# Optimization experiments

Measured on AMD Instinct MI355X. Metric: run time of the kernel, lower is better.

Reference implementation:

```python
import jax, jax.numpy as jnp
import numpy as np
import math

B, T, C, H = 2, 2048, 1024, 16
D = C // H

def setup_inputs() -> dict:
    key = jax.random.key(0)
    ks = jax.random.split(key, 10)
    s = 1.0 / math.sqrt(C)
    return {
        "x": jax.random.normal(ks[0], (B, T, C), jnp.float32),
        "x_query": jax.random.normal(ks[1], (B, T, C), jnp.float32),
        "Wq": jax.random.normal(ks[2], (C, C), jnp.float32) * s,
        "bq": jax.random.normal(ks[3], (C,), jnp.float32) * 0.02,
        "Wk": jax.random.normal(ks[4], (C, C), jnp.float32) * s,
        "bk": jax.random.normal(ks[5], (C,), jnp.float32) * 0.02,
        "Wv": jax.random.normal(ks[6], (C, C), jnp.float32) * s,
        "bv": jax.random.normal(ks[7], (C,), jnp.float32) * 0.02,
        "Wp": jax.random.normal(ks[8], (C, C), jnp.float32) * s,
        "bp": jax.random.normal(ks[9], (C,), jnp.float32) * 0.02,
    }

def reference(x, x_query, Wq, bq, Wk, bk, Wv, bv, Wp, bp):
    # torch nn.Linear: y = x @ W^T + b
    Tq = x_query.shape[1]
    Tk = x.shape[1]
    q = (x_query @ Wq.T + bq).reshape(B, Tq, H, D).transpose(0, 2, 1, 3)  # [B,H,Tq,D]
    k = (x @ Wk.T + bk).reshape(B, Tk, H, D).transpose(0, 2, 1, 3)       # [B,H,Tk,D]
    v = (x @ Wv.T + bv).reshape(B, Tk, H, D).transpose(0, 2, 1, 3)       # [B,H,Tk,D]
    scale = 1.0 / math.sqrt(D)
    att = jnp.einsum('bhqd,bhkd->bhqk', q, k) * scale                    # [B,H,Tq,Tk]
    # use_mask=True, past_kv=None -> causal tril mask over (Tq, Tk)
    mask = jnp.tril(jnp.ones((Tq, Tk), dtype=bool))
    att = jnp.where(mask[None, None, :, :], att, -jnp.inf)
    att = jax.nn.softmax(att, axis=-1)
    y = jnp.einsum('bhqk,bhkd->bhqd', att, v)                            # [B,H,Tq,D]
    y = y.transpose(0, 2, 1, 3).reshape(B, Tq, C)
    y = y @ Wp.T + bp
    return y
```

## Files before the change

### kernel.cpp

```cpp
#include <hip/hip_runtime.h>

typedef __bf16 bf16;
typedef __attribute__((ext_vector_type(8))) __bf16 bf16x8;
typedef __attribute__((ext_vector_type(4))) float f32x4;
typedef __attribute__((ext_vector_type(16))) float f32x16;
typedef __attribute__((ext_vector_type(4))) unsigned u32x4;

#define MFMA16(a, b, c) __builtin_amdgcn_mfma_f32_16x16x32_bf16((a), (b), (c), 0, 0, 0)
#define MFMA32(a, b, c) __builtin_amdgcn_mfma_f32_32x32x16_bf16((a), (b), (c), 0, 0, 0)
#define NEG_BIG (-1e30f)
#define SCL_LOG2 0.18033688011112042f

__device__ __forceinline__ void gload_lds16(void* lds, const void* g) {
  __builtin_amdgcn_global_load_lds(
      (const __attribute__((address_space(1))) void*)g,
      (__attribute__((address_space(3))) void*)lds, 16, 0, 0);
}

__device__ __forceinline__ unsigned pk2(float x, float y) {
  const unsigned short a = __builtin_bit_cast(unsigned short, (bf16)x);
  const unsigned short b = __builtin_bit_cast(unsigned short, (bf16)y);
  return (unsigned)a | ((unsigned)b << 16);
}

__global__ void cvt6(const float* __restrict__ s0, const float* __restrict__ s1,
                     const float* __restrict__ s2, const float* __restrict__ s3,
                     const float* __restrict__ s4, const float* __restrict__ s5,
                     bf16* __restrict__ d0, bf16* __restrict__ d1,
                     bf16* __restrict__ d2, bf16* __restrict__ d3,
                     bf16* __restrict__ d4, bf16* __restrict__ d5) {
  const int c = blockIdx.x * blockDim.x + threadIdx.x;
  if (c >= 1572864) return;
  const float* s; bf16* d; int off;
  if (c < 524288)        { s = s0; d = d0; off = c; }
  else if (c < 1048576)  { s = s1; d = d1; off = c - 524288; }
  else {
    const int c2 = c - 1048576, seg = c2 >> 17;
    off = c2 & 131071;
    s = seg == 0 ? s2 : seg == 1 ? s3 : seg == 2 ? s4 : s5;
    d = seg == 0 ? d2 : seg == 1 ? d3 : seg == 2 ? d4 : d5;
  }
  const float4 a = ((const float4*)s)[off * 2 + 0];
  const float4 b = ((const float4*)s)[off * 2 + 1];
  bf16x8 o;
  o[0] = (bf16)a.x; o[1] = (bf16)a.y; o[2] = (bf16)a.z; o[3] = (bf16)a.w;
  o[4] = (bf16)b.x; o[5] = (bf16)b.y; o[6] = (bf16)b.z; o[7] = (bf16)b.w;
  ((bf16x8*)d)[off] = o;
}

__global__ void gemm_qkv(const bf16* __restrict__ XQ, const bf16* __restrict__ X,
                         const bf16* __restrict__ Wq, const bf16* __restrict__ Wk,
                         const bf16* __restrict__ Wv,
                         const float* __restrict__ bq, const float* __restrict__ bk,
                         const float* __restrict__ bv,
                         bf16* __restrict__ Qo, bf16* __restrict__ Ko,
                         bf16* __restrict__ Vto) {
  __shared__ __align__(16) bf16 As[128 * 32];
  __shared__ __align__(16) bf16 Bs[128 * 32];
  const int tid = threadIdx.x;
  const int wv = tid >> 6, lane = tid & 63;
  const int wr = wv >> 1, wc = wv & 1;
  const int lr = lane & 15, lg = lane >> 4;
  const int seg = blockIdx.x >> 3;
  const int n0 = (blockIdx.x & 7) * 128;
  const int m0 = blockIdx.y * 128;
  const bf16* __restrict__ A = seg == 0 ? XQ : X;
  const bf16* __restrict__ W = seg == 0 ? Wq : seg == 1 ? Wk : Wv;
  const float* __restrict__ bias = seg == 0 ? bq : seg == 1 ? bk : bv;
  const int K = 1024;

  f32x4 acc[4][4] = {};

  for (int k0 = 0; k0 < K; k0 += 32) {
    __syncthreads();
#pragma unroll
    for (int j = 0; j < 2; ++j) {
      const int e8 = (j * 256 + tid) * 8;
      const int row = e8 >> 5, col = e8 & 31;
      gload_lds16(As + (size_t)(j * 256 + wv * 64) * 8,
                  A + (size_t)(m0 + row) * K + k0 + col);
      gload_lds16(Bs + (size_t)(j * 256 + wv * 64) * 8,
                  W + (size_t)(n0 + row) * K + k0 + col);
    }
    __syncthreads();
    bf16x8 af[4], bfr[4];
#pragma unroll
    for (int i = 0; i < 4; ++i)
      af[i] = *(const bf16x8*)&As[(wr * 64 + i * 16 + lr) * 32 + lg * 8];
#pragma unroll
    for (int j = 0; j < 4; ++j)
      bfr[j] = *(const bf16x8*)&Bs[(wc * 64 + j * 16 + lr) * 32 + lg * 8];
#pragma unroll
    for (int i = 0; i < 4; ++i)
#pragma unroll
      for (int j = 0; j < 4; ++j)
        acc[i][j] = MFMA16(af[i], bfr[j], acc[i][j]);
  }

#pragma unroll
  for (int j = 0; j < 4; ++j) {
    const int n = n0 + wc * 64 + j * 16 + lr;
    const float bvv = bias[n];
    const int h = n >> 6, d = n & 63;
#pragma unroll
    for (int i = 0; i < 4; ++i) {
#pragma unroll
      for (int r = 0; r < 4; ++r) {
        const int m = m0 + wr * 64 + i * 16 + lg * 4 + r;
        const float v = acc[i][j][r] + bvv;
        const int b = m >> 11, t = m & 2047;
        if (seg == 0)      Qo[((size_t)(b * 16 + h) * 2048 + t) * 64 + d] = (bf16)v;
        else if (seg == 1) Ko[((size_t)(b * 16 + h) * 2048 + t) * 64 + d] = (bf16)v;
        else               Vto[((size_t)(b * 16 + h) * 64 + d) * 2048 + t] = (bf16)v;
      }
    }
  }
}

template <int BN>
__global__ void gemm_out(const bf16* __restrict__ A, const bf16* __restrict__ W,
                         const float* __restrict__ bias, float* __restrict__ out,
                         int M, int N, int K) {
  __shared__ __align__(16) bf16 As[128 * 32];
  __shared__ __align__(16) bf16 Bs[BN * 32];
  constexpr int NF = BN / 32;
  const int tid = threadIdx.x;
  const int wv = tid >> 6, lane = tid & 63;
  const int wr = wv >> 1, wc = wv & 1;
  const int lr = lane & 15, lg = lane >> 4;
  const int m0 = blockIdx.y * 128, n0 = blockIdx.x * BN;

  f32x4 acc[4][NF] = {};

  for (int k0 = 0; k0 < K; k0 += 32) {
    __syncthreads();
#pragma unroll
    for (int j = 0; j < 2; ++j) {
      const int e8 = (j * 256 + tid) * 8;
      const int row = e8 >> 5, col = e8 & 31;
      gload_lds16(As + (size_t)(j * 256 + wv * 64) * 8,
                  A + (size_t)(m0 + row) * K + k0 + col);
    }
#pragma unroll
    for (int j = 0; j < BN / 64; ++j) {
      const int e8 = (j * 256 + tid) * 8;
      const int row = e8 >> 5, col = e8 & 31;
      gload_lds16(Bs + (size_t)(j * 256 + wv * 64) * 8,
                  W + (size_t)(n0 + row) * K + k0 + col);
    }
    __syncthreads();
    bf16x8 af[4], bfr[NF];
#pragma unroll
    for (int i = 0; i < 4; ++i)
      af[i] = *(const bf16x8*)&As[(wr * 64 + i * 16 + lr) * 32 + lg * 8];
#pragma unroll
    for (int j = 0; j < NF; ++j)
      bfr[j] = *(const bf16x8*)&Bs[(wc * (BN / 2) + j * 16 + lr) * 32 + lg * 8];
#pragma unroll
    for (int i = 0; i < 4; ++i)
#pragma unroll
      for (int j = 0; j < NF; ++j)
        acc[i][j] = MFMA16(af[i], bfr[j], acc[i][j]);
  }

#pragma unroll
  for (int j = 0; j < NF; ++j) {
    const int n = n0 + wc * (BN / 2) + j * 16 + lr;
    const float bv = bias[n];
#pragma unroll
    for (int i = 0; i < 4; ++i) {
#pragma unroll
      for (int r = 0; r < 4; ++r) {
        const int m = m0 + wr * 64 + i * 16 + lg * 4 + r;
        out[(size_t)m * N + n] = acc[i][j][r] + bv;
      }
    }
  }
}

__global__ void attn_fwd(const bf16* __restrict__ Q, const bf16* __restrict__ Kk,
                         const bf16* __restrict__ Vt, bf16* __restrict__ attout) {
  __shared__ __align__(16) char Ks[2][8192];
  __shared__ __align__(16) char Vs[2][8192];

  const int tid = threadIdx.x;
  const int wv = tid >> 6, lane = tid & 63;
  const int q31 = lane & 31, hi = lane >> 5, l7 = lane & 7;
  const int bid = blockIdx.x;
  const int qt = (bid < 256) ? (15 - (bid >> 5)) : ((bid - 256) >> 5);
  const int bh = bid & 31;
  const int q0 = qt * 128;
  const int qs = q0 + wv * 32;
  const int qa = qs + q31;
  const size_t bhT = (size_t)bh * 2048;
  const bf16* Vh = Vt + (size_t)bh * 64 * 2048;

  bf16x8 qf[4];
#pragma unroll
  for (int kw = 0; kw < 4; ++kw)
    qf[kw] = *(const bf16x8*)(Q + (bhT + qa) * 64 + kw * 16 + hi * 8);

  f32x16 O0 = {}, O1 = {};
  float m2 = NEG_BIG, l = 0.f;

  const int nt = q0 / 64 + 2;

  auto STAGE = [&](int buf, int kv0) {
#pragma unroll
    for (int rr = 0; rr < 2; ++rr) {
      const int c = rr * 256 + tid;
      const int row = c >> 3, cc = c & 7;
      const int gcol = (cc ^ (row & 7)) * 8;
      gload_lds16(Ks[buf] + (rr * 256 + wv * 64) * 16,
                  Kk + (bhT + kv0 + row) * 64 + gcol);
      gload_lds16(Vs[buf] + (rr * 256 + wv * 64) * 16,
                  Vh + (size_t)row * 2048 + kv0 + gcol);
    }
  };

  int cur = 0;
  STAGE(0, 0);
  __syncthreads();

  for (int it = 0; it < nt; ++it) {
    const int kv0 = it * 64;
    if (it + 1 < nt) STAGE(cur ^ 1, (it + 1) * 64);

    if (kv0 <= qs + 31) {
      f32x16 S0 = {}, S1 = {};
      __builtin_amdgcn_s_setprio(1);
#pragma unroll
      for (int kw = 0; kw < 4; ++kw) {
        const int cb = (32 * kw + 16 * hi) ^ (l7 << 4);
        const bf16x8 k0 = *(const bf16x8*)(Ks[cur] + q31 * 128 + cb);
        const bf16x8 k1 = *(const bf16x8*)(Ks[cur] + (32 + q31) * 128 + cb);
        S0 = MFMA32(k0, qf[kw], S0);
        S1 = MFMA32(k1, qf[kw], S1);
      }
      __builtin_amdgcn_s_setprio(0);

      float p[32];
#pragma unroll
      for (int r = 0; r < 16; ++r) {
        p[r]      = S0[r] * SCL_LOG2;
        p[16 + r] = S1[r] * SCL_LOG2;
      }
      if (kv0 + 63 > qs) {
#pragma unroll
        for (int a = 0; a < 2; ++a)
#pragma unroll
          for (int r = 0; r < 16; ++r) {
            const int kva = kv0 + a * 32 + (r & 3) + 8 * (r >> 2) + 4 * hi;
            if (kva > qa) p[a * 16 + r] = NEG_BIG;
          }
      }

      float w16[16];
#pragma unroll
      for (int i = 0; i < 16; ++i) w16[i] = fmaxf(p[i], p[i + 16]);
#pragma unroll
      for (int i = 0; i < 8; ++i) w16[i] = fmaxf(w16[i], w16[i + 8]);
#pragma unroll
      for (int i = 0; i < 4; ++i) w16[i] = fmaxf(w16[i], w16[i + 4]);
      float mx = fmaxf(fmaxf(w16[0], w16[1]), fmaxf(w16[2], w16[3]));
      mx = fmaxf(mx, __shfl_xor(mx, 32));
      if (!__all(mx - m2 <= 8.f)) {
        const float mnew = fmaxf(m2, mx);
        const float fac = exp2f(m2 - mnew);
        l *= fac;
#pragma unroll
        for (int r = 0; r < 16; ++r) { O0[r] *= fac; O1[r] *= fac; }
        m2 = mnew;
      }
#pragma unroll
      for (int i = 0; i < 32; ++i) p[i] = exp2f(p[i] - m2);
      float s16[16];
#pragma unroll
      for (int i = 0; i < 16; ++i) s16[i] = p[i] + p[i + 16];
#pragma unroll
      for (int i = 0; i < 8; ++i) s16[i] += s16[i + 8];
#pragma unroll
      for (int i = 0; i < 4; ++i) s16[i] += s16[i + 4];
      float rs = (s16[0] + s16[1]) + (s16[2] + s16[3]);
      rs += __shfl_xor(rs, 32);
      l += rs;

      bf16x8 pf[4];
#pragma unroll
      for (int ks = 0; ks < 4; ++ks) {
        const int base = 16 * (ks >> 1) + 8 * (ks & 1);
        const unsigned g0 = pk2(p[base + 0], p[base + 1]);
        const unsigned g1 = pk2(p[base + 2], p[base + 3]);
        const unsigned g2 = pk2(p[base + 4], p[base + 5]);
        const unsigned g3 = pk2(p[base + 6], p[base + 7]);
        const unsigned e0 = __shfl_xor(hi ? g0 : g2, 32);
        const unsigned e1 = __shfl_xor(hi ? g1 : g3, 32);
        u32x4 w4;
        w4[0] = hi ? e0 : g0;
        w4[1] = hi ? e1 : g1;
        w4[2] = hi ? g2 : e0;
        w4[3] = hi ? g3 : e1;
        pf[ks] = __builtin_bit_cast(bf16x8, w4);
      }

      __builtin_amdgcn_s_setprio(1);
#pragma unroll
      for (int ks = 0; ks < 4; ++ks) {
        const int cb = (32 * ks + 16 * hi) ^ (l7 << 4);
        const bf16x8 v0 = *(const bf16x8*)(Vs[cur] + q31 * 128 + cb);
        const bf16x8 v1 = *(const bf16x8*)(Vs[cur] + (32 + q31) * 128 + cb);
        O0 = MFMA32(v0, pf[ks], O0);
        O1 = MFMA32(v1, pf[ks], O1);
      }
      __builtin_amdgcn_s_setprio(0);
    }
    __syncthreads();
    cur ^= 1;
  }

  const int b = bh >> 4, h = bh & 15;
  const float inv = 1.f / l;
  bf16* orow = attout + ((size_t)b * 2048 + qa) * 1024 + h * 64;
#pragma unroll
  for (int r = 0; r < 16; ++r) {
    const int dd = (r & 3) + 8 * (r >> 2) + 4 * hi;
    orow[dd]      = (bf16)(O0[r] * inv);
    orow[32 + dd] = (bf16)(O1[r] * inv);
  }
}

extern "C" void kernel_launch(void* const* d_in, const int* in_sizes, int n_in,
                              void* d_out, int out_size, void* d_ws, size_t ws_size,
                              hipStream_t stream) {
  const float* x   = (const float*)d_in[0];
  const float* xq  = (const float*)d_in[1];
  const float* Wq  = (const float*)d_in[2];
  const float* bq  = (const float*)d_in[3];
  const float* Wk  = (const float*)d_in[4];
  const float* bk  = (const float*)d_in[5];
  const float* Wv  = (const float*)d_in[6];
  const float* bv  = (const float*)d_in[7];
  const float* Wp  = (const float*)d_in[8];
  const float* bp  = (const float*)d_in[9];
  float* out = (float*)d_out;

  const size_t NTC = 4194304;
  const size_t NW  = 1048576;
  bf16* ws = (bf16*)d_ws;
  bf16* XQb = ws;
  bf16* Xb  = XQb + NTC;
  bf16* Wqb = Xb + NTC;
  bf16* Wkb = Wqb + NW;
  bf16* Wvb = Wkb + NW;
  bf16* Wpb = Wvb + NW;
  bf16* Qw  = Wpb + NW;
  bf16* Kw  = Qw + NTC;
  bf16* Vtw = Kw + NTC;
  bf16* Aw  = Vtw + NTC;

  dim3 blk(256);
  cvt6<<<dim3(6144), blk, 0, stream>>>(xq, x, Wq, Wk, Wv, Wp,
                                       XQb, Xb, Wqb, Wkb, Wvb, Wpb);
  gemm_qkv<<<dim3(24, 32), blk, 0, stream>>>(XQb, Xb, Wqb, Wkb, Wvb,
                                             bq, bk, bv, Qw, Kw, Vtw);
  attn_fwd<<<dim3(512), blk, 0, stream>>>(Qw, Kw, Vtw, Aw);
  gemm_out<64><<<dim3(16, 32), blk, 0, stream>>>(Aw, Wpb, bp, out, 4096, 1024, 1024);
}
```

Before: 144.5 us.

## Split KV range for long causal query tiles and add combine kernel

Query tiles 8–15, which have the longest causal KV ranges, now run as two blocks that each cover half of the KV tiles. Each half writes unnormalized fp32 partial outputs plus its running max and sum to workspace. A new attn_combine kernel merges the two halves with log-sum-exp weights and writes bf16. The goal is to shorten the critical path of the longest attention blocks and spread work more evenly over 768 blocks. The cost is an extra kernel launch and an fp32 round trip through memory, and the partials reuse workspace that held the converted inputs.

New measurement: 141.3 us. 1.02x faster.

```diff
diff --git a/kernel.cpp b/kernel.cpp
--- a/kernel.cpp
+++ b/kernel.cpp
@@ -179,16 +179,27 @@
 }
 
 __global__ void attn_fwd(const bf16* __restrict__ Q, const bf16* __restrict__ Kk,
-                         const bf16* __restrict__ Vt, bf16* __restrict__ attout) {
+                         const bf16* __restrict__ Vt, bf16* __restrict__ attout,
+                         float* __restrict__ Opart, float* __restrict__ Ml) {
   __shared__ __align__(16) char Ks[2][8192];
   __shared__ __align__(16) char Vs[2][8192];
 
   const int tid = threadIdx.x;
   const int wv = tid >> 6, lane = tid & 63;
   const int q31 = lane & 31, hi = lane >> 5, l7 = lane & 7;
-  const int bid = blockIdx.x;
-  const int qt = (bid < 256) ? (15 - (bid >> 5)) : ((bid - 256) >> 5);
-  const int bh = bid & 31;
+  const int g = blockIdx.x >> 5, bh = blockIdx.x & 31;
+  int qt, t0, t1;
+  const bool split = g < 16;
+  if (split) {
+    qt = 15 - (g >> 1);
+    const int nt = 2 * qt + 2, hh = nt >> 1;
+    t0 = (g & 1) ? hh : 0;
+    t1 = (g & 1) ? nt : hh;
+  } else {
+    qt = 23 - g;
+    t0 = 0;
+    t1 = 2 * qt + 2;
+  }
   const int q0 = qt * 128;
   const int qs = q0 + wv * 32;
   const int qa = qs + q31;
@@ -202,8 +213,6 @@
 
   f32x16 O0 = {}, O1 = {};
   float m2 = NEG_BIG, l = 0.f;
-
-  const int nt = q0 / 64 + 2;
 
   auto STAGE = [&](int buf, int kv0) {
 #pragma unroll
@@ -218,13 +227,13 @@
     }
   };
 
-  int cur = 0;
-  STAGE(0, 0);
+  STAGE(0, t0 * 64);
   __syncthreads();
 
-  for (int it = 0; it < nt; ++it) {
+  for (int it = t0; it < t1; ++it) {
     const int kv0 = it * 64;
-    if (it + 1 < nt) STAGE(cur ^ 1, (it + 1) * 64);
+    const int cur = (it - t0) & 1;
+    if (it + 1 < t1) STAGE(cur ^ 1, (it + 1) * 64);
 
     if (kv0 <= qs + 31) {
       f32x16 S0 = {}, S1 = {};
@@ -315,17 +324,58 @@
       __builtin_amdgcn_s_setprio(0);
     }
     __syncthreads();
-    cur ^= 1;
-  }
-
-  const int b = bh >> 4, h = bh & 15;
-  const float inv = 1.f / l;
-  bf16* orow = attout + ((size_t)b * 2048 + qa) * 1024 + h * 64;
-#pragma unroll
-  for (int r = 0; r < 16; ++r) {
-    const int dd = (r & 3) + 8 * (r >> 2) + 4 * hi;
-    orow[dd]      = (bf16)(O0[r] * inv);
-    orow[32 + dd] = (bf16)(O1[r] * inv);
+  }
+
+  if (!split) {
+    const int b = bh >> 4, h = bh & 15;
+    const float inv = 1.f / l;
+    bf16* orow = attout + ((size_t)b * 2048 + qa) * 1024 + h * 64;
+#pragma unroll
+    for (int r = 0; r < 16; ++r) {
+      const int dd = (r & 3) + 8 * (r >> 2) + 4 * hi;
+      orow[dd]      = (bf16)(O0[r] * inv);
+      orow[32 + dd] = (bf16)(O1[r] * inv);
+    }
+  } else {
+    const int pi = ((bh * 8 + (qt - 8)) * 2 + (g & 1));
+    float* Po = Opart + (size_t)pi * 8192;
+    const int row = wv * 32 + q31;
+#pragma unroll
+    for (int r = 0; r < 16; ++r) {
+      const int dd = (r & 3) + 8 * (r >> 2) + 4 * hi;
+      Po[row * 64 + dd]      = O0[r];
+      Po[row * 64 + 32 + dd] = O1[r];
+    }
+    Ml[pi * 256 + row]       = m2;
+    Ml[pi * 256 + 128 + row] = l;
+  }
+}
+
+__global__ void attn_combine(const float* __restrict__ Opart,
+                             const float* __restrict__ Ml,
+                             bf16* __restrict__ attout) {
+  const int u = blockIdx.x;
+  const int bh = u >> 3, qtu = u & 7;
+  const int pi0 = (bh * 8 + qtu) * 2;
+  const int tid = threadIdx.x;
+  const int row = tid >> 1, c0 = (tid & 1) * 32;
+  const float m1 = Ml[pi0 * 256 + row],       l1 = Ml[pi0 * 256 + 128 + row];
+  const float m2 = Ml[(pi0 + 1) * 256 + row], l2 = Ml[(pi0 + 1) * 256 + 128 + row];
+  const float M = fmaxf(m1, m2);
+  const float w1 = exp2f(m1 - M), w2 = exp2f(m2 - M);
+  const float inv = 1.f / (w1 * l1 + w2 * l2);
+  const float* p1 = Opart + (size_t)pi0 * 8192 + row * 64 + c0;
+  const float* p2 = Opart + (size_t)(pi0 + 1) * 8192 + row * 64 + c0;
+  const int b = bh >> 4, h = bh & 15, t = (qtu + 8) * 128 + row;
+  bf16* dst = attout + ((size_t)b * 2048 + t) * 1024 + h * 64 + c0;
+#pragma unroll
+  for (int d = 0; d < 32; d += 4) {
+    const float4 a = *(const float4*)(p1 + d);
+    const float4 bb = *(const float4*)(p2 + d);
+    dst[d + 0] = (bf16)((w1 * a.x + w2 * bb.x) * inv);
+    dst[d + 1] = (bf16)((w1 * a.y + w2 * bb.y) * inv);
+    dst[d + 2] = (bf16)((w1 * a.z + w2 * bb.z) * inv);
+    dst[d + 3] = (bf16)((w1 * a.w + w2 * bb.w) * inv);
   }
 }
 
@@ -357,12 +407,15 @@
   bf16* Kw  = Qw + NTC;
   bf16* Vtw = Kw + NTC;
   bf16* Aw  = Vtw + NTC;
+  float* Opart = (float*)d_ws;
+  float* Ml    = (float*)(Aw + NTC);
 
   dim3 blk(256);
   cvt6<<<dim3(6144), blk, 0, stream>>>(xq, x, Wq, Wk, Wv, Wp,
                                        XQb, Xb, Wqb, Wkb, Wvb, Wpb);
   gemm_qkv<<<dim3(24, 32), blk, 0, stream>>>(XQb, Xb, Wqb, Wkb, Wvb,
                                              bq, bk, bv, Qw, Kw, Vtw);
-  attn_fwd<<<dim3(512), blk, 0, stream>>>(Qw, Kw, Vtw, Aw);
+  attn_fwd<<<dim3(768), blk, 0, stream>>>(Qw, Kw, Vtw, Aw, Opart, Ml);
+  attn_combine<<<dim3(256), blk, 0, stream>>>(Opart, Ml, Aw);
   gemm_out<64><<<dim3(16, 32), blk, 0, stream>>>(Aw, Wpb, bp, out, 4096, 1024, 1024);
 }
```

## Split long causal attention tiles across KV segments with a combine pass

Applied to the files above, without the earlier changes.

Query tiles with long causal KV ranges are split into 2 or 3 KV segments, taken from a static schedule table, so the causal workload is spread more evenly over twice as many blocks. Split blocks write unnormalized partial outputs plus row max and sum to workspace, and a new combine kernel merges them with log-sum-exp weighting. The row sum is now computed by an extra MFMA against a ones vector instead of shuffle reductions, and the scale is folded into the exp2 argument with an FMA. The partials reuse the front of the workspace, which held the already-consumed converted inputs. The cost is an extra kernel launch and extra global traffic for the partials.

New measurement: 128.2 us. 1.13x faster.

```diff
diff --git a/kernel.cpp b/kernel.cpp
--- a/kernel.cpp
+++ b/kernel.cpp
@@ -10,6 +10,7 @@
 #define MFMA32(a, b, c) __builtin_amdgcn_mfma_f32_32x32x16_bf16((a), (b), (c), 0, 0, 0)
 #define NEG_BIG (-1e30f)
 #define SCL_LOG2 0.18033688011112042f
+#define THR_RAW 44.3614195558365f
 
 __device__ __forceinline__ void gload_lds16(void* lds, const void* g) {
   __builtin_amdgcn_global_load_lds(
@@ -22,6 +23,13 @@
   const unsigned short b = __builtin_bit_cast(unsigned short, (bf16)y);
   return (unsigned)a | ((unsigned)b << 16);
 }
+
+static __device__ const signed char KQT[32] =
+  {15,15,10,10, 15,14,14,14,13, 9, 9, 4, 13,13,12,12, 8, 8,
+   12,11,11,11, 7, 7, 3,  6, 6,  5, 5, 2,  1,  0};
+static __device__ const signed char KSEG[32] =
+  { 0, 1, 0, 1,  2, 0, 1, 2, 0, 0, 1, 0,  1, 2, 0, 1, 0, 1,
+    2, 0, 1, 2, 0, 1, 0,  0, 1,  0, 1, 0,  0,  0};
 
 __global__ void cvt6(const float* __restrict__ s0, const float* __restrict__ s1,
                      const float* __restrict__ s2, const float* __restrict__ s3,
@@ -179,16 +187,21 @@
 }
 
 __global__ void attn_fwd(const bf16* __restrict__ Q, const bf16* __restrict__ Kk,
-                         const bf16* __restrict__ Vt, bf16* __restrict__ attout) {
+                         const bf16* __restrict__ Vt, bf16* __restrict__ attout,
+                         bf16* __restrict__ Opart, float* __restrict__ Ml) {
   __shared__ __align__(16) char Ks[2][8192];
   __shared__ __align__(16) char Vs[2][8192];
 
   const int tid = threadIdx.x;
   const int wv = tid >> 6, lane = tid & 63;
   const int q31 = lane & 31, hi = lane >> 5, l7 = lane & 7;
-  const int bid = blockIdx.x;
-  const int qt = (bid < 256) ? (15 - (bid >> 5)) : ((bid - 256) >> 5);
-  const int bh = bid & 31;
+  const int kind = blockIdx.x >> 5, bh = blockIdx.x & 31;
+  const int qt = KQT[kind], seg = KSEG[kind];
+  const int nt = 2 * qt + 2;
+  const int ns = qt >= 11 ? 3 : (qt >= 5 ? 2 : 1);
+  const int t0 = (nt * seg) / ns, t1 = (nt * (seg + 1)) / ns;
+  const bool split = ns > 1;
+
   const int q0 = qt * 128;
   const int qs = q0 + wv * 32;
   const int qa = qs + q31;
@@ -200,10 +213,12 @@
   for (int kw = 0; kw < 4; ++kw)
     qf[kw] = *(const bf16x8*)(Q + (bhT + qa) * 64 + kw * 16 + hi * 8);
 
+  u32x4 onesu; onesu[0] = onesu[1] = onesu[2] = onesu[3] = 0x3F803F80u;
+  const bf16x8 ones8 = __builtin_bit_cast(bf16x8, onesu);
+
   f32x16 O0 = {}, O1 = {};
-  float m2 = NEG_BIG, l = 0.f;
-
-  const int nt = q0 / 64 + 2;
+  f32x16 Ol = {};
+  float m2 = NEG_BIG;
 
   auto STAGE = [&](int buf, int kv0) {
 #pragma unroll
@@ -218,13 +233,13 @@
     }
   };
 
-  int cur = 0;
-  STAGE(0, 0);
+  STAGE(0, t0 * 64);
   __syncthreads();
 
-  for (int it = 0; it < nt; ++it) {
+  for (int it = t0; it < t1; ++it) {
     const int kv0 = it * 64;
-    if (it + 1 < nt) STAGE(cur ^ 1, (it + 1) * 64);
+    const int cur = (it - t0) & 1;
+    if (it + 1 < t1) STAGE(cur ^ 1, (it + 1) * 64);
 
     if (kv0 <= qs + 31) {
       f32x16 S0 = {}, S1 = {};
@@ -241,10 +256,7 @@
 
       float p[32];
 #pragma unroll
-      for (int r = 0; r < 16; ++r) {
-        p[r]      = S0[r] * SCL_LOG2;
-        p[16 + r] = S1[r] * SCL_LOG2;
-      }
+      for (int r = 0; r < 16; ++r) { p[r] = S0[r]; p[16 + r] = S1[r]; }
       if (kv0 + 63 > qs) {
 #pragma unroll
         for (int a = 0; a < 2; ++a)
@@ -264,26 +276,17 @@
       for (int i = 0; i < 4; ++i) w16[i] = fmaxf(w16[i], w16[i + 4]);
       float mx = fmaxf(fmaxf(w16[0], w16[1]), fmaxf(w16[2], w16[3]));
       mx = fmaxf(mx, __shfl_xor(mx, 32));
-      if (!__all(mx - m2 <= 8.f)) {
+      if (!__all(mx - m2 <= THR_RAW)) {
         const float mnew = fmaxf(m2, mx);
-        const float fac = exp2f(m2 - mnew);
-        l *= fac;
+        const float fac = exp2f((m2 - mnew) * SCL_LOG2);
 #pragma unroll
         for (int r = 0; r < 16; ++r) { O0[r] *= fac; O1[r] *= fac; }
+        Ol[0] *= fac;
         m2 = mnew;
       }
-#pragma unroll
-      for (int i = 0; i < 32; ++i) p[i] = exp2f(p[i] - m2);
-      float s16[16];
-#pragma unroll
-      for (int i = 0; i < 16; ++i) s16[i] = p[i] + p[i + 16];
-#pragma unroll
-      for (int i = 0; i < 8; ++i) s16[i] += s16[i + 8];
-#pragma unroll
-      for (int i = 0; i < 4; ++i) s16[i] += s16[i + 4];
-      float rs = (s16[0] + s16[1]) + (s16[2] + s16[3]);
-      rs += __shfl_xor(rs, 32);
-      l += rs;
+      const float nm2 = -m2 * SCL_LOG2;
+#pragma unroll
+      for (int i = 0; i < 32; ++i) p[i] = exp2f(__builtin_fmaf(p[i], SCL_LOG2, nm2));
 
       bf16x8 pf[4];
 #pragma unroll
@@ -311,22 +314,88 @@
         const bf16x8 v1 = *(const bf16x8*)(Vs[cur] + (32 + q31) * 128 + cb);
         O0 = MFMA32(v0, pf[ks], O0);
         O1 = MFMA32(v1, pf[ks], O1);
+        Ol = MFMA32(ones8, pf[ks], Ol);
       }
       __builtin_amdgcn_s_setprio(0);
     }
     __syncthreads();
-    cur ^= 1;
-  }
-
-  const int b = bh >> 4, h = bh & 15;
-  const float inv = 1.f / l;
-  bf16* orow = attout + ((size_t)b * 2048 + qa) * 1024 + h * 64;
-#pragma unroll
-  for (int r = 0; r < 16; ++r) {
-    const int dd = (r & 3) + 8 * (r >> 2) + 4 * hi;
-    orow[dd]      = (bf16)(O0[r] * inv);
-    orow[32 + dd] = (bf16)(O1[r] * inv);
-  }
+  }
+
+  const float l = Ol[0];
+  if (!split) {
+    const int b = bh >> 4, h = bh & 15;
+    const float inv = 1.f / l;
+    bf16* orow = attout + ((size_t)b * 2048 + qa) * 1024 + h * 64;
+#pragma unroll
+    for (int r = 0; r < 16; ++r) {
+      const int dd = (r & 3) + 8 * (r >> 2) + 4 * hi;
+      orow[dd]      = (bf16)(O0[r] * inv);
+      orow[32 + dd] = (bf16)(O1[r] * inv);
+    }
+  } else {
+    const int sbase = (qt < 11) ? (qt - 5) * 2 : 12 + (qt - 11) * 3;
+    const int slot = bh * 27 + sbase + seg;
+    bf16* Po = Opart + (size_t)slot * 8192;
+    const int row = wv * 32 + q31;
+#pragma unroll
+    for (int r = 0; r < 16; ++r) {
+      const int dd = (r & 3) + 8 * (r >> 2) + 4 * hi;
+      Po[row * 64 + dd]      = (bf16)O0[r];
+      Po[row * 64 + 32 + dd] = (bf16)O1[r];
+    }
+    Ml[slot * 256 + row]       = m2;
+    Ml[slot * 256 + 128 + row] = l;
+  }
+}
+
+__global__ void attn_combine(const bf16* __restrict__ Opart,
+                             const float* __restrict__ Ml,
+                             bf16* __restrict__ attout) {
+  const int u = blockIdx.x;
+  const int bh = u / 11, qti = u - bh * 11;
+  const int qt = qti + 5;
+  const int ns = qt >= 11 ? 3 : 2;
+  const int sbase = (qt < 11) ? (qt - 5) * 2 : 12 + (qt - 11) * 3;
+  const int s0 = bh * 27 + sbase;
+  const int tid = threadIdx.x;
+  const int row = tid >> 1, c0 = (tid & 1) * 32;
+
+  float m[3], lv[3];
+  float M = NEG_BIG;
+#pragma unroll
+  for (int s = 0; s < 3; ++s)
+    if (s < ns) {
+      m[s] = Ml[(s0 + s) * 256 + row];
+      lv[s] = Ml[(s0 + s) * 256 + 128 + row];
+      M = fmaxf(M, m[s]);
+    }
+  float w[3], L = 0.f;
+#pragma unroll
+  for (int s = 0; s < 3; ++s)
+    if (s < ns) {
+      w[s] = exp2f((m[s] - M) * SCL_LOG2);
+      L += w[s] * lv[s];
+    }
+  const float inv = 1.f / L;
+
+  float acc[32] = {};
+#pragma unroll
+  for (int s = 0; s < 3; ++s)
+    if (s < ns) {
+      const bf16* p = Opart + (size_t)(s0 + s) * 8192 + row * 64 + c0;
+      const float ws = w[s];
+#pragma unroll
+      for (int j = 0; j < 4; ++j) {
+        const bf16x8 v = *(const bf16x8*)(p + j * 8);
+#pragma unroll
+        for (int e = 0; e < 8; ++e) acc[j * 8 + e] += ws * (float)v[e];
+      }
+    }
+
+  const int b = bh >> 4, h = bh & 15, t = qt * 128 + row;
+  bf16* dst = attout + ((size_t)b * 2048 + t) * 1024 + h * 64 + c0;
+#pragma unroll
+  for (int d = 0; d < 32; ++d) dst[d] = (bf16)(acc[d] * inv);
 }
 
 extern "C" void kernel_launch(void* const* d_in, const int* in_sizes, int n_in,
@@ -357,12 +426,15 @@
   bf16* Kw  = Qw + NTC;
   bf16* Vtw = Kw + NTC;
   bf16* Aw  = Vtw + NTC;
+  bf16* Opart = (bf16*)d_ws;
+  float* Ml   = (float*)(Aw + NTC);
 
   dim3 blk(256);
   cvt6<<<dim3(6144), blk, 0, stream>>>(xq, x, Wq, Wk, Wv, Wp,
                                        XQb, Xb, Wqb, Wkb, Wvb, Wpb);
   gemm_qkv<<<dim3(24, 32), blk, 0, stream>>>(XQb, Xb, Wqb, Wkb, Wvb,
                                              bq, bk, bv, Qw, Kw, Vtw);
-  attn_fwd<<<dim3(512), blk, 0, stream>>>(Qw, Kw, Vtw, Aw);
+  attn_fwd<<<dim3(1024), blk, 0, stream>>>(Qw, Kw, Vtw, Aw, Opart, Ml);
+  attn_combine<<<dim3(352), blk, 0, stream>>>(Opart, Ml, Aw);
   gemm_out<64><<<dim3(16, 32), blk, 0, stream>>>(Aw, Wpb, bp, out, 4096, 1024, 1024);
 }
```
